# Kernel tuning notes

Hardware: AMD Instinct MI355X
Metric: run time of the kernel (lower is better)

## Reference

```python
import jax, jax.numpy as jnp
import numpy as np

B, S, D, H = 2, 2048, 2048, 16
NEG = -1e9


def setup_inputs() -> dict:
    key = jax.random.key(0)
    ks = jax.random.split(key, 5)
    x = jax.random.normal(ks[0], (B, S, D), dtype=jnp.float32)
    # additive causal mask: 0 on/below diagonal, -1e9 above
    causal = jnp.triu(jnp.full((S, S), NEG, dtype=jnp.float32), k=1)
    attn_mask = causal[None, None, :, :]  # [1,1,S,S]
    scale = 0.02
    Wq = jax.random.normal(ks[1], (D, D), dtype=jnp.float32) * scale
    Wk = jax.random.normal(ks[2], (D, D), dtype=jnp.float32) * scale
    Wv = jax.random.normal(ks[3], (D, D), dtype=jnp.float32) * scale
    Wo = jax.random.normal(ks[4], (D, D), dtype=jnp.float32) * scale
    return {"x": x, "attn_mask": attn_mask, "Wq": Wq, "Wk": Wk, "Wv": Wv, "Wo": Wo}


def reference(x, attn_mask, Wq, Wk, Wv, Wo):
    b, s, hidden = x.shape
    d = hidden // H
    # torch nn.Linear: y = x @ W.T (no bias since bias=None)
    q = (x @ Wq.T).reshape(b, s, H, d).transpose(0, 2, 1, 3)  # [b,h,s,d]
    k = (x @ Wk.T).reshape(b, s, H, d).transpose(0, 2, 1, 3)
    v = (x @ Wv.T).reshape(b, s, H, d).transpose(0, 2, 1, 3)
    q = q * (1.0 / float(d) ** 0.5)
    att = jnp.einsum("bhqd,bhkd->bhqk", q, k) + attn_mask  # [b,h,s,s]
    att = jax.nn.softmax(att.astype(jnp.float32), axis=-1).astype(x.dtype)
    y = jnp.einsum("bhqk,bhkd->bhqd", att, v)
    y = y.transpose(0, 2, 1, 3).reshape(b, s, hidden)
    return y @ Wo.T
```

## Files before the change

### kernel.cpp

```cpp
#include <hip/hip_runtime.h>
#include <hip/hip_bf16.h>
#include <cstdint>
#include <cstddef>

typedef __bf16 bf16;
typedef __bf16 bf16x8 __attribute__((ext_vector_type(8)));
typedef __bf16 bf16x4 __attribute__((ext_vector_type(4)));
typedef float f32x4 __attribute__((ext_vector_type(4)));

static constexpr int BATCH = 2;
static constexpr int SEQ = 2048;
static constexpr int DMODEL = 2048;
static constexpr int NH = 16;
static constexpr int HD = 128;
static constexpr int MROWS = BATCH * SEQ;

#define GLOBAL_AS(p) ((const __attribute__((address_space(1))) void*)(p))
#define LDS_AS(p)    ((__attribute__((address_space(3))) void*)(p))
#define WAIT_VMCNT0() __builtin_amdgcn_s_waitcnt(0x0F70)

__global__ void cvt5_kernel(const float* __restrict__ x,
                            const float* __restrict__ wq, const float* __restrict__ wk,
                            const float* __restrict__ wv, const float* __restrict__ wo,
                            bf16* __restrict__ dst) {
  const int i = blockIdx.x * blockDim.x + threadIdx.x;
  const float* src;
  int local;
  if (i < 2097152) { src = x; local = i; }
  else {
    const int r = i - 2097152;
    const int w = r >> 20;
    local = r & 1048575;
    src = (w == 0) ? wq : (w == 1) ? wk : (w == 2) ? wv : wo;
  }
  float4 f = reinterpret_cast<const float4*>(src)[local];
  bf16x4 o;
  o.x = (bf16)f.x; o.y = (bf16)f.y; o.z = (bf16)f.z; o.w = (bf16)f.w;
  reinterpret_cast<bf16x4*>(dst)[i] = o;
}

enum { MODE_QKV = 0, MODE_OUT = 1 };

template <int MODE>
__global__ __launch_bounds__(256, 4) void gemm_bt(
    const bf16* __restrict__ A, const bf16* __restrict__ W,
    bf16* __restrict__ Oq, bf16* __restrict__ Ok, bf16* __restrict__ Ov,
    float* __restrict__ Oout) {
  constexpr int Kd = DMODEL;
  __shared__ __align__(16) bf16 As[128][64];
  __shared__ __align__(16) bf16 Bs[128][64];
  const int n0 = blockIdx.x * 128;
  const int m0 = blockIdx.y * 128;
  const int tid = threadIdx.x;
  const int wave = tid >> 6;
  const int lane = tid & 63;
  const int quad = lane >> 4;
  const int l16 = lane & 15;
  const int wm = (wave >> 1) * 64;
  const int wn = (wave & 1) * 64;
  const int srow = lane >> 3;
  const int schunk = ((lane & 7) - srow) & 7;

  f32x4 acc[4][4] = {};
  for (int kt = 0; kt < Kd; kt += 64) {
#pragma unroll
    for (int i = 0; i < 4; i++) {
      const int r = wave * 32 + i * 8;
      __builtin_amdgcn_global_load_lds(
          GLOBAL_AS(&A[(size_t)(m0 + r + srow) * Kd + kt + schunk * 8]),
          LDS_AS(&As[r][0]), 16, 0, 0);
      __builtin_amdgcn_global_load_lds(
          GLOBAL_AS(&W[(size_t)(n0 + r + srow) * Kd + kt + schunk * 8]),
          LDS_AS(&Bs[r][0]), 16, 0, 0);
    }
    WAIT_VMCNT0();
    __syncthreads();
#pragma unroll
    for (int ks = 0; ks < 2; ks++) {
      const int col = (((ks * 4 + quad + l16) & 7)) * 8;
      bf16x8 af[4], bfr[4];
#pragma unroll
      for (int t = 0; t < 4; t++)
        af[t] = *reinterpret_cast<const bf16x8*>(&As[wm + t * 16 + l16][col]);
#pragma unroll
      for (int t = 0; t < 4; t++)
        bfr[t] = *reinterpret_cast<const bf16x8*>(&Bs[wn + t * 16 + l16][col]);
#pragma unroll
      for (int tm = 0; tm < 4; tm++)
#pragma unroll
        for (int tn = 0; tn < 4; tn++)
          acc[tm][tn] = __builtin_amdgcn_mfma_f32_16x16x32_bf16(af[tm], bfr[tn], acc[tm][tn], 0, 0, 0);
    }
    __syncthreads();
  }
#pragma unroll
  for (int tm = 0; tm < 4; tm++) {
#pragma unroll
    for (int tn = 0; tn < 4; tn++) {
      const int row0 = m0 + wm + tm * 16 + quad * 4;
      if constexpr (MODE == MODE_OUT) {
        const int col = n0 + wn + tn * 16 + l16;
#pragma unroll
        for (int j = 0; j < 4; j++)
          Oout[(size_t)(row0 + j) * DMODEL + col] = acc[tm][tn][j];
      } else {
        const int mat = n0 >> 11;
        const int col = (n0 & 2047) + wn + tn * 16 + l16;
        const int h = col >> 7, dd = col & 127;
        if (mat == 2) {
          const int b = row0 >> 11, s = row0 & 2047;
          bf16x4 pk;
#pragma unroll
          for (int j = 0; j < 4; j++) pk[j] = (bf16)acc[tm][tn][j];
          *reinterpret_cast<bf16x4*>(&Ov[((size_t)(b * NH + h) * HD + dd) * SEQ + s]) = pk;
        } else {
          bf16* O = mat ? Ok : Oq;
          const float scale = mat ? 1.0f : 0.08838834764831845f;
#pragma unroll
          for (int j = 0; j < 4; j++) {
            const int row = row0 + j;
            const int b = row >> 11, s = row & 2047;
            O[((size_t)(b * NH + h) * SEQ + s) * HD + dd] = (bf16)(acc[tm][tn][j] * scale);
          }
        }
      }
    }
  }
}

__global__ __launch_bounds__(256, 2) void attn_kernel(
    const bf16* __restrict__ Q, const bf16* __restrict__ K,
    const bf16* __restrict__ Vt, bf16* __restrict__ Y) {
  const int j = blockIdx.x;
  const int bh = blockIdx.y;
  __shared__ __align__(16) char smem[58368];
  auto Ks  = (bf16(*)[64][128])smem;
  auto Vts = (bf16(*)[64])(smem + 32768);
  auto Ps  = (bf16(*)[16][72])(smem + 49152);
  const int tid = threadIdx.x;
  const int wave = tid >> 6;
  const int lane = tid & 63;
  const int quad = lane >> 4;
  const int l16 = lane & 15;

  const bf16* Kbh = K + (size_t)bh * SEQ * HD;
  const bf16* Vbh = Vt + (size_t)bh * HD * SEQ;
  const int b = bh >> 4, h = bh & 15;

  const int krow = lane >> 4;
  const int kphys = lane & 15;
  const int vrow = lane >> 3;
  const int vphys = lane & 7;
  const int vchunk = (vphys - vrow) & 7;

  for (int pass = 0; pass < 2; ++pass) {
    const int qt = pass ? (31 - j) : j;
    const int q0 = qt * 64;
    const int ntiles = qt + 1;

    const bf16* Qw = Q + ((size_t)bh * SEQ + q0 + wave * 16) * HD;
    bf16x8 qf[4];
#pragma unroll
    for (int kk = 0; kk < 4; kk++)
      qf[kk] = *reinterpret_cast<const bf16x8*>(&Qw[(size_t)l16 * HD + kk * 32 + quad * 8]);

    f32x4 oacc[8] = {};
    float m_i = -3.0e38f, l_i = 0.f;

    __syncthreads();
#pragma unroll
    for (int i = 0; i < 4; i++) {
      const int rbase = wave * 16 + i * 4;
      const int c = ((kphys - krow - i * 4) & 15);
      __builtin_amdgcn_global_load_lds(
          GLOBAL_AS(&Kbh[(size_t)(rbase + krow) * HD + c * 8]),
          LDS_AS(&Ks[0][rbase][0]), 16, 0, 0);
    }

    for (int t = 0; t < ntiles; ++t) {
      const int kt = t * 64;
      const int X = t & 1;
      WAIT_VMCNT0();
      __syncthreads();

#pragma unroll
      for (int i = 0; i < 4; i++) {
        const int rbase = wave * 32 + i * 8;
        __builtin_amdgcn_global_load_lds(
            GLOBAL_AS(&Vbh[(size_t)(rbase + vrow) * SEQ + kt + vchunk * 8]),
            LDS_AS(&Vts[rbase][0]), 16, 0, 0);
      }

      f32x4 sacc[4] = {};
#pragma unroll
      for (int kk = 0; kk < 4; kk++) {
        const int kcol = (((kk * 4 + quad + l16) & 15)) * 8;
        bf16x8 ka[4];
#pragma unroll
        for (int mt = 0; mt < 4; mt++)
          ka[mt] = *reinterpret_cast<const bf16x8*>(&Ks[X][mt * 16 + l16][kcol]);
#pragma unroll
        for (int mt = 0; mt < 4; mt++)
          sacc[mt] = __builtin_amdgcn_mfma_f32_16x16x32_bf16(ka[mt], qf[kk], sacc[mt], 0, 0, 0);
      }

      const int qg_loc = wave * 16 + l16;
      float mx = -3.0e38f;
      if (t == ntiles - 1) {
#pragma unroll
        for (int mt = 0; mt < 4; mt++)
#pragma unroll
          for (int jj = 0; jj < 4; jj++) {
            const int kg = mt * 16 + quad * 4 + jj;
            float v = (kg <= qg_loc) ? sacc[mt][jj] : -3.0e38f;
            sacc[mt][jj] = v;
            mx = fmaxf(mx, v);
          }
      } else {
#pragma unroll
        for (int mt = 0; mt < 4; mt++)
#pragma unroll
          for (int jj = 0; jj < 4; jj++) mx = fmaxf(mx, sacc[mt][jj]);
      }
      mx = fmaxf(mx, __shfl_xor(mx, 16));
      mx = fmaxf(mx, __shfl_xor(mx, 32));
      const float mnew = fmaxf(m_i, mx);
      const float alpha = __expf(m_i - mnew);
      m_i = mnew;
      float rs = 0.f;
#pragma unroll
      for (int mt = 0; mt < 4; mt++)
#pragma unroll
        for (int jj = 0; jj < 4; jj++) {
          float p = __expf(sacc[mt][jj] - mnew);
          sacc[mt][jj] = p;
          rs += p;
        }
      rs += __shfl_xor(rs, 16);
      rs += __shfl_xor(rs, 32);
      l_i = l_i * alpha + rs;
#pragma unroll
      for (int mt8 = 0; mt8 < 8; mt8++)
#pragma unroll
        for (int jj = 0; jj < 4; jj++) oacc[mt8][jj] *= alpha;

#pragma unroll
      for (int mt = 0; mt < 4; mt++) {
        bf16x4 pk;
#pragma unroll
        for (int jj = 0; jj < 4; jj++) pk[jj] = (bf16)sacc[mt][jj];
        *reinterpret_cast<bf16x4*>(&Ps[wave][l16][mt * 16 + quad * 4]) = pk;
      }

      WAIT_VMCNT0();
      __syncthreads();

      if (t + 1 < ntiles) {
        const int ktn = kt + 64;
#pragma unroll
        for (int i = 0; i < 4; i++) {
          const int rbase = wave * 16 + i * 4;
          const int c = ((kphys - krow - i * 4) & 15);
          __builtin_amdgcn_global_load_lds(
              GLOBAL_AS(&Kbh[(size_t)(ktn + rbase + krow) * HD + c * 8]),
              LDS_AS(&Ks[1 - X][rbase][0]), 16, 0, 0);
        }
      }

#pragma unroll
      for (int kk2 = 0; kk2 < 2; kk2++) {
        const int vcol = ((kk2 * 4 + quad + l16) & 7) * 8;
        bf16x8 pb = *reinterpret_cast<const bf16x8*>(&Ps[wave][l16][kk2 * 32 + quad * 8]);
#pragma unroll
        for (int mt8 = 0; mt8 < 8; mt8++) {
          bf16x8 av = *reinterpret_cast<const bf16x8*>(&Vts[mt8 * 16 + l16][vcol]);
          oacc[mt8] = __builtin_amdgcn_mfma_f32_16x16x32_bf16(av, pb, oacc[mt8], 0, 0, 0);
        }
      }
    }

    const float inv = 1.0f / l_i;
    const int qg = q0 + wave * 16 + l16;
#pragma unroll
    for (int mt8 = 0; mt8 < 8; mt8++) {
      bf16x4 pk;
#pragma unroll
      for (int jj = 0; jj < 4; jj++) pk[jj] = (bf16)(oacc[mt8][jj] * inv);
      *reinterpret_cast<bf16x4*>(
          &Y[(size_t)(b * SEQ + qg) * DMODEL + h * HD + mt8 * 16 + quad * 4]) = pk;
    }
  }
}

extern "C" void kernel_launch(void* const* d_in, const int* in_sizes, int n_in,
                              void* d_out, int out_size, void* d_ws, size_t ws_size,
                              hipStream_t stream) {
  const float* x  = (const float*)d_in[0];
  const float* Wq = (const float*)d_in[2];
  const float* Wk = (const float*)d_in[3];
  const float* Wv = (const float*)d_in[4];
  const float* Wo = (const float*)d_in[5];
  float* out = (float*)d_out;

  char* ws = (char*)d_ws;
  bf16* xb  = (bf16*)(ws + 0);
  bf16* Wqb = (bf16*)(ws + 16777216);
  bf16* Wob = (bf16*)(ws + 41943040);
  bf16* Qb  = (bf16*)(ws + 50331648);
  bf16* Kb  = (bf16*)(ws + 67108864);
  bf16* Vtb = (bf16*)(ws + 83886080);
  bf16* Yb  = xb;
  if (ws_size < 100663296) return;

  cvt5_kernel<<<24576, 256, 0, stream>>>(x, Wq, Wk, Wv, Wo, xb);

  gemm_bt<MODE_QKV><<<dim3(48, MROWS / 128), 256, 0, stream>>>(
      xb, Wqb, Qb, Kb, Vtb, nullptr);

  attn_kernel<<<dim3(16, BATCH * NH), 256, 0, stream>>>(Qb, Kb, Vtb, Yb);

  gemm_bt<MODE_OUT><<<dim3(16, MROWS / 128), 256, 0, stream>>>(
      Yb, Wob, nullptr, nullptr, nullptr, out);
}
```

Before: 368.5 us.

## Double attention query tile to 128 rows with two subtiles per wave

Each attention block now processes 128 query rows, with each wave handling two 16-row subtiles that share the same K and V tiles loaded into LDS. This halves K/V staging traffic and barrier count per query row and raises MFMA work per LDS read. The P buffer becomes a per-wave swizzled 32x64 layout to avoid bank conflicts. In exchange, accumulator register pressure doubles and the grid halves to 256 blocks, reducing occupancy and latency hiding.

```diff
diff --git a/kernel.cpp b/kernel.cpp
--- a/kernel.cpp
+++ b/kernel.cpp
@@ -133,15 +133,16 @@
     const bf16* __restrict__ Vt, bf16* __restrict__ Y) {
   const int j = blockIdx.x;
   const int bh = blockIdx.y;
-  __shared__ __align__(16) char smem[58368];
+  __shared__ __align__(16) char smem[65536];
   auto Ks  = (bf16(*)[64][128])smem;
   auto Vts = (bf16(*)[64])(smem + 32768);
-  auto Ps  = (bf16(*)[16][72])(smem + 49152);
+  char* PsW;
   const int tid = threadIdx.x;
   const int wave = tid >> 6;
   const int lane = tid & 63;
   const int quad = lane >> 4;
   const int l16 = lane & 15;
+  PsW = smem + 49152 + wave * 4096;
 
   const bf16* Kbh = K + (size_t)bh * SEQ * HD;
   const bf16* Vbh = Vt + (size_t)bh * HD * SEQ;
@@ -154,18 +155,22 @@
   const int vchunk = (vphys - vrow) & 7;
 
   for (int pass = 0; pass < 2; ++pass) {
-    const int qt = pass ? (31 - j) : j;
-    const int q0 = qt * 64;
-    const int ntiles = qt + 1;
-
-    const bf16* Qw = Q + ((size_t)bh * SEQ + q0 + wave * 16) * HD;
-    bf16x8 qf[4];
-#pragma unroll
-    for (int kk = 0; kk < 4; kk++)
-      qf[kk] = *reinterpret_cast<const bf16x8*>(&Qw[(size_t)l16 * HD + kk * 32 + quad * 8]);
-
-    f32x4 oacc[8] = {};
-    float m_i = -3.0e38f, l_i = 0.f;
+    const int qt = pass ? (15 - j) : j;
+    const int q0 = qt * 128;
+    const int ntiles = 2 * qt + 2;
+
+    const bf16* Qw = Q + ((size_t)bh * SEQ + q0 + wave * 32) * HD;
+    bf16x8 qf[2][4];
+#pragma unroll
+    for (int nt = 0; nt < 2; nt++)
+#pragma unroll
+      for (int kk = 0; kk < 4; kk++)
+        qf[nt][kk] = *reinterpret_cast<const bf16x8*>(
+            &Qw[(size_t)(nt * 16 + l16) * HD + kk * 32 + quad * 8]);
+
+    f32x4 oacc[8][2] = {};
+    float m_i[2] = {-3.0e38f, -3.0e38f};
+    float l_i[2] = {0.f, 0.f};
 
     __syncthreads();
 #pragma unroll
@@ -191,7 +196,7 @@
             LDS_AS(&Vts[rbase][0]), 16, 0, 0);
       }
 
-      f32x4 sacc[4] = {};
+      f32x4 sacc[4][2] = {};
 #pragma unroll
       for (int kk = 0; kk < 4; kk++) {
         const int kcol = (((kk * 4 + quad + l16) & 15)) * 8;
@@ -201,55 +206,63 @@
           ka[mt] = *reinterpret_cast<const bf16x8*>(&Ks[X][mt * 16 + l16][kcol]);
 #pragma unroll
         for (int mt = 0; mt < 4; mt++)
-          sacc[mt] = __builtin_amdgcn_mfma_f32_16x16x32_bf16(ka[mt], qf[kk], sacc[mt], 0, 0, 0);
-      }
-
-      const int qg_loc = wave * 16 + l16;
-      float mx = -3.0e38f;
-      if (t == ntiles - 1) {
+#pragma unroll
+          for (int nt = 0; nt < 2; nt++)
+            sacc[mt][nt] = __builtin_amdgcn_mfma_f32_16x16x32_bf16(ka[mt], qf[nt][kk], sacc[mt][nt], 0, 0, 0);
+      }
+
+      const bool mask_tile = (t >= ntiles - 2);
+#pragma unroll
+      for (int nt = 0; nt < 2; nt++) {
+        const int qg = q0 + wave * 32 + nt * 16 + l16;
+        float mx = -3.0e38f;
+        if (mask_tile) {
+#pragma unroll
+          for (int mt = 0; mt < 4; mt++)
+#pragma unroll
+            for (int jj = 0; jj < 4; jj++) {
+              const int kg = kt + mt * 16 + quad * 4 + jj;
+              float v = (kg <= qg) ? sacc[mt][nt][jj] : -3.0e38f;
+              sacc[mt][nt][jj] = v;
+              mx = fmaxf(mx, v);
+            }
+        } else {
+#pragma unroll
+          for (int mt = 0; mt < 4; mt++)
+#pragma unroll
+            for (int jj = 0; jj < 4; jj++) mx = fmaxf(mx, sacc[mt][nt][jj]);
+        }
+        mx = fmaxf(mx, __shfl_xor(mx, 16));
+        mx = fmaxf(mx, __shfl_xor(mx, 32));
+        const float mnew = fmaxf(m_i[nt], mx);
+        const float alpha = __expf(m_i[nt] - mnew);
+        m_i[nt] = mnew;
+        float rs = 0.f;
 #pragma unroll
         for (int mt = 0; mt < 4; mt++)
 #pragma unroll
           for (int jj = 0; jj < 4; jj++) {
-            const int kg = mt * 16 + quad * 4 + jj;
-            float v = (kg <= qg_loc) ? sacc[mt][jj] : -3.0e38f;
-            sacc[mt][jj] = v;
-            mx = fmaxf(mx, v);
+            float p = __expf(sacc[mt][nt][jj] - mnew);
+            sacc[mt][nt][jj] = p;
+            rs += p;
           }
-      } else {
-#pragma unroll
-        for (int mt = 0; mt < 4; mt++)
-#pragma unroll
-          for (int jj = 0; jj < 4; jj++) mx = fmaxf(mx, sacc[mt][jj]);
-      }
-      mx = fmaxf(mx, __shfl_xor(mx, 16));
-      mx = fmaxf(mx, __shfl_xor(mx, 32));
-      const float mnew = fmaxf(m_i, mx);
-      const float alpha = __expf(m_i - mnew);
-      m_i = mnew;
-      float rs = 0.f;
-#pragma unroll
-      for (int mt = 0; mt < 4; mt++)
-#pragma unroll
-        for (int jj = 0; jj < 4; jj++) {
-          float p = __expf(sacc[mt][jj] - mnew);
-          sacc[mt][jj] = p;
-          rs += p;
-        }
-      rs += __shfl_xor(rs, 16);
-      rs += __shfl_xor(rs, 32);
-      l_i = l_i * alpha + rs;
-#pragma unroll
-      for (int mt8 = 0; mt8 < 8; mt8++)
-#pragma unroll
-        for (int jj = 0; jj < 4; jj++) oacc[mt8][jj] *= alpha;
-
-#pragma unroll
-      for (int mt = 0; mt < 4; mt++) {
-        bf16x4 pk;
-#pragma unroll
-        for (int jj = 0; jj < 4; jj++) pk[jj] = (bf16)sacc[mt][jj];
-        *reinterpret_cast<bf16x4*>(&Ps[wave][l16][mt * 16 + quad * 4]) = pk;
+        rs += __shfl_xor(rs, 16);
+        rs += __shfl_xor(rs, 32);
+        l_i[nt] = l_i[nt] * alpha + rs;
+#pragma unroll
+        for (int mt8 = 0; mt8 < 8; mt8++)
+#pragma unroll
+          for (int jj = 0; jj < 4; jj++) oacc[mt8][nt][jj] *= alpha;
+
+#pragma unroll
+        for (int mt = 0; mt < 4; mt++) {
+          bf16x4 pk;
+#pragma unroll
+          for (int jj = 0; jj < 4; jj++) pk[jj] = (bf16)sacc[mt][nt][jj];
+          const int row = nt * 16 + l16;
+          const int ph = (mt * 2 + (quad >> 1) + row) & 7;
+          *reinterpret_cast<bf16x4*>(&PsW[row * 128 + ph * 16 + (quad & 1) * 8]) = pk;
+        }
       }
 
       WAIT_VMCNT0();
@@ -269,25 +282,36 @@
 
 #pragma unroll
       for (int kk2 = 0; kk2 < 2; kk2++) {
+        bf16x8 pb[2];
+#pragma unroll
+        for (int nt = 0; nt < 2; nt++) {
+          const int row = nt * 16 + l16;
+          const int ph = (kk2 * 4 + quad + row) & 7;
+          pb[nt] = *reinterpret_cast<const bf16x8*>(&PsW[row * 128 + ph * 16]);
+        }
         const int vcol = ((kk2 * 4 + quad + l16) & 7) * 8;
-        bf16x8 pb = *reinterpret_cast<const bf16x8*>(&Ps[wave][l16][kk2 * 32 + quad * 8]);
 #pragma unroll
         for (int mt8 = 0; mt8 < 8; mt8++) {
           bf16x8 av = *reinterpret_cast<const bf16x8*>(&Vts[mt8 * 16 + l16][vcol]);
-          oacc[mt8] = __builtin_amdgcn_mfma_f32_16x16x32_bf16(av, pb, oacc[mt8], 0, 0, 0);
-        }
-      }
-    }
-
-    const float inv = 1.0f / l_i;
-    const int qg = q0 + wave * 16 + l16;
-#pragma unroll
-    for (int mt8 = 0; mt8 < 8; mt8++) {
-      bf16x4 pk;
-#pragma unroll
-      for (int jj = 0; jj < 4; jj++) pk[jj] = (bf16)(oacc[mt8][jj] * inv);
-      *reinterpret_cast<bf16x4*>(
-          &Y[(size_t)(b * SEQ + qg) * DMODEL + h * HD + mt8 * 16 + quad * 4]) = pk;
+#pragma unroll
+          for (int nt = 0; nt < 2; nt++)
+            oacc[mt8][nt] = __builtin_amdgcn_mfma_f32_16x16x32_bf16(av, pb[nt], oacc[mt8][nt], 0, 0, 0);
+        }
+      }
+    }
+
+#pragma unroll
+    for (int nt = 0; nt < 2; nt++) {
+      const float inv = 1.0f / l_i[nt];
+      const int qg = q0 + wave * 32 + nt * 16 + l16;
+#pragma unroll
+      for (int mt8 = 0; mt8 < 8; mt8++) {
+        bf16x4 pk;
+#pragma unroll
+        for (int jj = 0; jj < 4; jj++) pk[jj] = (bf16)(oacc[mt8][nt][jj] * inv);
+        *reinterpret_cast<bf16x4*>(
+            &Y[(size_t)(b * SEQ + qg) * DMODEL + h * HD + mt8 * 16 + quad * 4]) = pk;
+      }
     }
   }
 }
@@ -317,7 +341,7 @@
   gemm_bt<MODE_QKV><<<dim3(48, MROWS / 128), 256, 0, stream>>>(
       xb, Wqb, Qb, Kb, Vtb, nullptr);
 
-  attn_kernel<<<dim3(16, BATCH * NH), 256, 0, stream>>>(Qb, Kb, Vtb, Yb);
+  attn_kernel<<<dim3(8, BATCH * NH), 256, 0, stream>>>(Qb, Kb, Vtb, Yb);
 
   gemm_bt<MODE_OUT><<<dim3(16, MROWS / 128), 256, 0, stream>>>(
       Yb, Wob, nullptr, nullptr, nullptr, out);
```

Measured after the change: 366.0 us. No clear change (-0.7%).
